# Performance work log

Hardware: AMD Instinct MI355X
Metric: run time of the kernel (lower is better)

The kernel has to match this reference:

```python
import jax, jax.numpy as jnp
import numpy as np

N = 100000        # nodes
E_RAND = 1600000  # random edges (self loops appended -> E = E_RAND + N)
H = 64            # agg_hidden
IN = 7            # in_channels
L = 3             # n_layer
FC = 128          # fc_hidden
C = 2             # num_classes
G = 256           # graphs in the batch
SLOPE = 0.2       # GATv2 LeakyReLU negative slope


def _gatv2(x, src, dst, Wl, bl, Wr, br, att, bias):
    # GATv2Conv, heads=1, concat=True, no edge_attr
    xl = x @ Wl.T + bl                                      # [N,H] source transform
    xr = x @ Wr.T + br                                      # [N,H] target transform
    e = jax.nn.leaky_relu(xl[src] + xr[dst], SLOPE) @ att   # [E] per-edge score
    m = jax.ops.segment_max(e, dst, num_segments=N)         # segment softmax over in-edges
    w = jnp.exp(e - m[dst])
    denom = jax.ops.segment_sum(w, dst, num_segments=N)
    alpha = w / denom[dst]                                  # self loops guarantee denom > 0
    out = jax.ops.segment_sum(alpha[:, None] * xl[src], dst, num_segments=N)
    return out + bias


def _forward(x, eps, m0, v0, mrest, vrest, fc1_W, fc1_b, fc2_W, fc2_b, edge_index, batch):
    src, dst = edge_index[0], edge_index[1]
    mean = jax.nn.elu(_gatv2(x, src, dst, *m0))
    log_var = jax.nn.elu(_gatv2(x, src, dst, *v0))
    for i in range(L - 1):  # dropout is a no-op in eval mode
        mean = jax.nn.elu(_gatv2(mean, src, dst, *[p[i] for p in mrest]))
        log_var = jax.nn.elu(_gatv2(log_var, src, dst, *[p[i] for p in vrest]))
    z = mean + eps * jnp.exp(0.5 * log_var)                 # reparameterize
    counts = jax.ops.segment_sum(jnp.ones((N,), z.dtype), batch, num_segments=G)
    zg = jax.ops.segment_sum(z, batch, num_segments=G) / counts[:, None]  # global_mean_pool
    h = jax.nn.relu(zg @ fc1_W.T + fc1_b)
    logits = h @ fc2_W.T + fc2_b
    return jax.nn.log_softmax(logits, axis=1), mean, log_var


def setup_inputs() -> dict:
    key = jax.random.key(0)
    ks = iter(jax.random.split(key, 48))

    def nrm(shape, s=0.1):
        return s * jax.random.normal(next(ks), shape, jnp.float32)

    x = jax.random.normal(next(ks), (N, IN), jnp.float32)
    src = jax.random.randint(next(ks), (E_RAND,), 0, N)
    dst = jax.random.randint(next(ks), (E_RAND,), 0, N)
    loops = jnp.arange(N)
    edge_index = jnp.stack([jnp.concatenate([src, loops]),
                            jnp.concatenate([dst, loops])])  # add_self_loops=True
    batch = jnp.sort(jax.random.randint(next(ks), (N,), 0, G))
    eps = jax.random.normal(next(ks), (N, H), jnp.float32)

    d = dict(x=x, eps=eps, edge_index=edge_index, batch=batch)
    for pre, din in (("m0", IN), ("v0", IN)):
        d[pre + "_Wl"] = nrm((H, din)); d[pre + "_bl"] = nrm((H,))
        d[pre + "_Wr"] = nrm((H, din)); d[pre + "_br"] = nrm((H,))
        d[pre + "_att"] = nrm((H,));    d[pre + "_bias"] = nrm((H,))
    for pre in ("m", "v"):  # stacked hidden layers [L-1, ...]
        d[pre + "_Wl"] = nrm((L - 1, H, H)); d[pre + "_bl"] = nrm((L - 1, H))
        d[pre + "_Wr"] = nrm((L - 1, H, H)); d[pre + "_br"] = nrm((L - 1, H))
        d[pre + "_att"] = nrm((L - 1, H));   d[pre + "_bias"] = nrm((L - 1, H))
    d["fc1_W"] = nrm((FC, H)); d["fc1_b"] = nrm((FC,))
    d["fc2_W"] = nrm((C, FC)); d["fc2_b"] = nrm((C,))
    return d


def reference(x, eps, edge_index, batch,
              m0_Wl, m0_bl, m0_Wr, m0_br, m0_att, m0_bias,
              v0_Wl, v0_bl, v0_Wr, v0_br, v0_att, v0_bias,
              m_Wl, m_bl, m_Wr, m_br, m_att, m_bias,
              v_Wl, v_bl, v_Wr, v_br, v_att, v_bias,
              fc1_W, fc1_b, fc2_W, fc2_b):
    m0 = (m0_Wl, m0_bl, m0_Wr, m0_br, m0_att, m0_bias)
    v0 = (v0_Wl, v0_bl, v0_Wr, v0_br, v0_att, v0_bias)
    mrest = (m_Wl, m_bl, m_Wr, m_br, m_att, m_bias)
    vrest = (v_Wl, v_bl, v_Wr, v_br, v_att, v_bias)
    return _forward(x, eps, m0, v0, mrest, vrest, fc1_W, fc1_b, fc2_W, fc2_b, edge_index, batch)
```

## Files before the change

kernel.cpp:

```cpp
#include <hip/hip_runtime.h>
#include <hip/hip_fp16.h>
#include <math.h>


#define BSH 7
#define BMSK ((1 << BSH) - 1)
#define CHUNK 4096
#define SNB 4096

typedef _Float16 h2 __attribute__((ext_vector_type(2)));
typedef _Float16 h8 __attribute__((ext_vector_type(8)));
typedef float f4 __attribute__((ext_vector_type(4)));

__device__ __forceinline__ float elu1(float v) {
    return v > 0.f ? v : (__expf(v) - 1.f);
}
__device__ __forceinline__ h2 lrelu2(h2 v) {
    int ai = (*(int*)&v) & 0x7FFF7FFF;
    h2 a = *(h2*)&ai;
    h2 c06 = {(_Float16)0.6f, (_Float16)0.6f};
    h2 c04 = {(_Float16)0.4f, (_Float16)0.4f};
    return v * c06 + a * c04;
}


__global__ void k_hist_bucket(const int* __restrict__ dst, int E,
                              int* __restrict__ bcnt, int nbk) {
    __shared__ int h[1024];
    for (int i = threadIdx.x; i < 1024; i += blockDim.x) h[i] = 0;
    __syncthreads();
    int stride = gridDim.x * blockDim.x;
    for (int e = blockIdx.x * blockDim.x + threadIdx.x; e < E; e += stride)
        atomicAdd(&h[dst[e] >> BSH], 1);
    __syncthreads();
    for (int i = threadIdx.x; i < nbk; i += blockDim.x)
        if (h[i]) atomicAdd(&bcnt[i], h[i]);
}

__global__ void k_scan_buckets(const int* __restrict__ bcnt, int nbk, int* __restrict__ boff) {
    __shared__ int sh[1024];
    int t = threadIdx.x;
    int v = (t < nbk) ? bcnt[t] : 0;
    sh[t] = v;
    __syncthreads();
    for (int o = 1; o < 1024; o <<= 1) {
        int u = (t >= o) ? sh[t - o] : 0;
        __syncthreads();
        sh[t] += u;
        __syncthreads();
    }
    if (t < nbk) boff[t] = sh[t] - v;
    if (t == nbk - 1) boff[nbk] = sh[t];
}

__global__ __launch_bounds__(256) void k_binfill(
    const int* __restrict__ src, const int* __restrict__ dst, int E,
    const int* __restrict__ boff, int* __restrict__ bfill, int* __restrict__ pairs) {
    __shared__ int h[1024];
    __shared__ int sbase[1024];
    int c0 = blockIdx.x * CHUNK;
    int c1 = min(c0 + CHUNK, E);
    for (int i = threadIdx.x; i < 1024; i += 256) h[i] = 0;
    __syncthreads();
    for (int e = c0 + threadIdx.x; e < c1; e += 256)
        atomicAdd(&h[dst[e] >> BSH], 1);
    __syncthreads();
    for (int i = threadIdx.x; i < 1024; i += 256) {
        int c = h[i];
        sbase[i] = c ? (boff[i] + atomicAdd(&bfill[i], c)) : 0;
        h[i] = 0;
    }
    __syncthreads();
    for (int e = c0 + threadIdx.x; e < c1; e += 256) {
        int d = dst[e];
        int b = d >> BSH;
        int off = atomicAdd(&h[b], 1);
        pairs[sbase[b] + off] = (src[e] << BSH) | (d & BMSK);
    }
}

__global__ __launch_bounds__(256) void k_bucket_csr(
    const int* __restrict__ pairs, const int* __restrict__ boff,
    int* __restrict__ rowptr, int* __restrict__ col, int N, int E) {
    __shared__ int deg[128], fill[128], scan[128], base[128];
    int b = blockIdx.x;
    int e0 = boff[b], e1 = boff[b + 1];
    int t = threadIdx.x;
    if (t < 128) { deg[t] = 0; fill[t] = 0; }
    __syncthreads();
    for (int i = e0 + t; i < e1; i += 256)
        atomicAdd(&deg[pairs[i] & BMSK], 1);
    __syncthreads();
    if (t < 128) scan[t] = deg[t];
    __syncthreads();
    for (int o = 1; o < 128; o <<= 1) {
        int u = (t >= o && t < 128) ? scan[t - o] : 0;
        __syncthreads();
        if (t < 128) scan[t] += u;
        __syncthreads();
    }
    if (t < 128) {
        int excl = e0 + scan[t] - deg[t];
        int node = (b << BSH) + t;
        if (node < N) rowptr[node] = excl;
        if (node == N - 1) rowptr[N] = E;
        base[t] = excl;
    }
    __syncthreads();
    for (int i = e0 + t; i < e1; i += 256) {
        int pk = pairs[i];
        int d = pk & BMSK;
        int pos = base[d] + atomicAdd(&fill[d], 1);
        col[pos] = ((unsigned)pk) >> BSH;
    }
}


__global__ __launch_bounds__(256) void k_deg_hist(const int* __restrict__ rowptr, int n,
                                                  int* __restrict__ bin_cnt,
                                                  int* __restrict__ blk_base) {
    __shared__ int h[256];
    h[threadIdx.x] = 0;
    __syncthreads();
    int b0 = blockIdx.x * SNB;
    int b1 = min(b0 + SNB, n);
    for (int i = b0 + threadIdx.x; i < b1; i += 256) {
        int d = 255 - min(rowptr[i + 1] - rowptr[i], 255);
        atomicAdd(&h[d], 1);
    }
    __syncthreads();
    int c = h[threadIdx.x];
    blk_base[blockIdx.x * 256 + threadIdx.x] = c ? atomicAdd(&bin_cnt[threadIdx.x], c) : 0;
}

__global__ void k_scan256(const int* __restrict__ bin_cnt, int* __restrict__ bin_off) {
    __shared__ int sh[256];
    int t = threadIdx.x;
    int v = bin_cnt[t];
    sh[t] = v;
    __syncthreads();
    for (int o = 1; o < 256; o <<= 1) {
        int u = (t >= o) ? sh[t - o] : 0;
        __syncthreads();
        sh[t] += u;
        __syncthreads();
    }
    bin_off[t] = sh[t] - v;
}

__global__ __launch_bounds__(256) void k_deg_scatter(const int* __restrict__ rowptr, int n,
                                                     const int* __restrict__ bin_off,
                                                     const int* __restrict__ blk_base,
                                                     int* __restrict__ nodeof) {
    __shared__ int h[256];
    h[threadIdx.x] = 0;
    __syncthreads();
    int b0 = blockIdx.x * SNB;
    int b1 = min(b0 + SNB, n);
    for (int i = b0 + threadIdx.x; i < b1; i += 256) {
        int d = 255 - min(rowptr[i + 1] - rowptr[i], 255);
        int my = atomicAdd(&h[d], 1);
        nodeof[bin_off[d] + blk_base[blockIdx.x * 256 + d] + my] = i;
    }
}


__global__ void k_transform7(const float* __restrict__ X,
                             const float* __restrict__ mWl, const float* __restrict__ mbl,
                             const float* __restrict__ mWr, const float* __restrict__ mbr,
                             const float* __restrict__ vWl, const float* __restrict__ vbl,
                             const float* __restrict__ vWr, const float* __restrict__ vbr,
                             __half* __restrict__ xlb, __half* __restrict__ xrb, int n) {
    int t = blockIdx.x * blockDim.x + threadIdx.x;
    int node = t >> 6;
    if (node >= n) return;
    int h = t & 63;
    float aml = mbl[h], amr = mbr[h], avl = vbl[h], avr = vbr[h];
#pragma unroll
    for (int k = 0; k < 7; ++k) {
        float xv = X[node * 7 + k];
        aml = fmaf(xv, mWl[h * 7 + k], aml);
        amr = fmaf(xv, mWr[h * 7 + k], amr);
        avl = fmaf(xv, vWl[h * 7 + k], avl);
        avr = fmaf(xv, vWr[h * 7 + k], avr);
    }
    size_t o = (size_t)node * 128;
    xlb[o + h] = __float2half(aml);
    xlb[o + 64 + h] = __float2half(avl);
    xrb[o + h] = __float2half(amr);
    xrb[o + 64 + h] = __float2half(avr);
}

__global__ __launch_bounds__(256) void k_transform_mfma2(
    const float* __restrict__ Xm, const float* __restrict__ Xv,
    const float* __restrict__ mWl, const float* __restrict__ mbl,
    const float* __restrict__ mWr, const float* __restrict__ mbr,
    const float* __restrict__ vWl, const float* __restrict__ vbl,
    const float* __restrict__ vWr, const float* __restrict__ vbr,
    __half* __restrict__ xlb, __half* __restrict__ xrb, int n) {
    int brn = blockIdx.y;
    const float* X  = brn ? Xv : Xm;
    const float* Wl = brn ? vWl : mWl;
    const float* bl = brn ? vbl : mbl;
    const float* Wr = brn ? vWr : mWr;
    const float* br = brn ? vbr : mbr;
    int base = brn * 64;

    __shared__ float biasLds[128];
    {
        int t = threadIdx.x;
        if (t < 64) biasLds[t] = bl[t];
        else if (t < 128) biasLds[t] = br[t - 64];
    }
    __syncthreads();
    int lane = threadIdx.x & 63;
    int l16 = lane & 15, lhi = lane >> 4;

    h8 aW[2][8];
    const float* Wp0 = Wl + (size_t)l16 * 64 + lhi * 8;
    const float* Wp1 = Wr + (size_t)l16 * 64 + lhi * 8;
#pragma unroll
    for (int tl = 0; tl < 4; ++tl) {
#pragma unroll
        for (int c = 0; c < 2; ++c) {
            const float* p0 = Wp0 + (size_t)tl * 16 * 64 + c * 32;
            const float* p1 = Wp1 + (size_t)tl * 16 * 64 + c * 32;
            float4 u0 = *(const float4*)p0, u1 = *(const float4*)(p0 + 4);
            float4 v0 = *(const float4*)p1, v1 = *(const float4*)(p1 + 4);
            h8 a0 = {(_Float16)u0.x, (_Float16)u0.y, (_Float16)u0.z, (_Float16)u0.w,
                     (_Float16)u1.x, (_Float16)u1.y, (_Float16)u1.z, (_Float16)u1.w};
            h8 a1 = {(_Float16)v0.x, (_Float16)v0.y, (_Float16)v0.z, (_Float16)v0.w,
                     (_Float16)v1.x, (_Float16)v1.y, (_Float16)v1.z, (_Float16)v1.w};
            aW[0][tl * 2 + c] = a0;
            aW[1][tl * 2 + c] = a1;
        }
    }

    int ntiles = (n + 15) >> 4;
    int wtile = blockIdx.x * 4 + (threadIdx.x >> 6);
    int wstride = gridDim.x * 4;
    for (int tile = wtile; tile < ntiles; tile += wstride) {
        int nb = tile * 16;
        int node = nb + l16;
        int nload = min(node, n - 1);
        h8 Bf[2];
#pragma unroll
        for (int c = 0; c < 2; ++c) {
            const float* p = X + (size_t)nload * 64 + c * 32 + lhi * 8;
            float4 u0 = *(const float4*)p, u1 = *(const float4*)(p + 4);
            h8 b = {(_Float16)u0.x, (_Float16)u0.y, (_Float16)u0.z, (_Float16)u0.w,
                    (_Float16)u1.x, (_Float16)u1.y, (_Float16)u1.z, (_Float16)u1.w};
            Bf[c] = b;
        }
        f4 acc[2][4];
#pragma unroll
        for (int m = 0; m < 2; ++m)
#pragma unroll
            for (int tl = 0; tl < 4; ++tl) {
                f4 a = {0.f, 0.f, 0.f, 0.f};
                a = __builtin_amdgcn_mfma_f32_16x16x32_f16(aW[m][tl * 2 + 0], Bf[0], a, 0, 0, 0);
                a = __builtin_amdgcn_mfma_f32_16x16x32_f16(aW[m][tl * 2 + 1], Bf[1], a, 0, 0, 0);
                acc[m][tl] = a;
            }
        if (node < n) {
#pragma unroll
            for (int m = 0; m < 2; ++m) {
                __half* op = (m ? xrb : xlb) + (size_t)node * 128 + base;
#pragma unroll
                for (int tl = 0; tl < 4; ++tl) {
                    float4 bb = *(const float4*)&biasLds[m * 64 + tl * 16 + 4 * lhi];
                    h2 lo = {(_Float16)(acc[m][tl][0] + bb.x), (_Float16)(acc[m][tl][1] + bb.y)};
                    h2 hi = {(_Float16)(acc[m][tl][2] + bb.z), (_Float16)(acc[m][tl][3] + bb.w)};
                    uint2 pk = {*(unsigned*)&lo, *(unsigned*)&hi};
                    *(uint2*)(op + tl * 16 + 4 * lhi) = pk;
                }
            }
        }
    }
}


__global__ __launch_bounds__(256) void k_aggregate2(
    const __half* __restrict__ xlb, const __half* __restrict__ xrb,
    const float* __restrict__ attm, const float* __restrict__ attv,
    const float* __restrict__ biasm, const float* __restrict__ biasv,
    const int* __restrict__ rowptr, const int* __restrict__ col,
    const int* __restrict__ nodeof,
    float* __restrict__ outm, float* __restrict__ outv, int n) {
    int t = blockIdx.x * blockDim.x + threadIdx.x;
    int gid = t >> 4;
    if (gid >= n) return;
    int node = nodeof[gid];
    int l = t & 15;
    int s = l & 7;
    bool isv = l >= 8;

    int4 xri = ((const int4*)(xrb + (size_t)node * 128))[l];
    h2 xr0 = *(h2*)&xri.x, xr1 = *(h2*)&xri.y, xr2 = *(h2*)&xri.z, xr3 = *(h2*)&xri.w;
    const float* ap = (isv ? attv : attm) + s * 8;
    float4 af0 = *(const float4*)ap, af1 = *(const float4*)(ap + 4);
    h2 a0 = {(_Float16)af0.x, (_Float16)af0.y}, a1 = {(_Float16)af0.z, (_Float16)af0.w};
    h2 a2 = {(_Float16)af1.x, (_Float16)af1.y}, a3 = {(_Float16)af1.z, (_Float16)af1.w};

    float ac0 = 0.f, ac1 = 0.f, ac2 = 0.f, ac3 = 0.f;
    float ac4 = 0.f, ac5 = 0.f, ac6 = 0.f, ac7 = 0.f;
    float ssum = 0.f;

    auto proc = [&](int4 qi) {
        h2 x0 = *(h2*)&qi.x, x1 = *(h2*)&qi.y, x2 = *(h2*)&qi.z, x3 = *(h2*)&qi.w;
        h2 p = lrelu2(x0 + xr0) * a0;
        p = lrelu2(x1 + xr1) * a1 + p;
        p = lrelu2(x2 + xr2) * a2 + p;
        p = lrelu2(x3 + xr3) * a3 + p;
        float sc = (float)p.x + (float)p.y;
        sc += __shfl_xor(sc, 1);
        sc += __shfl_xor(sc, 2);
        sc += __shfl_xor(sc, 4);
        float w = __expf(sc);
        ssum += w;
        ac0 = fmaf(w, (float)x0.x, ac0);
        ac1 = fmaf(w, (float)x0.y, ac1);
        ac2 = fmaf(w, (float)x1.x, ac2);
        ac3 = fmaf(w, (float)x1.y, ac3);
        ac4 = fmaf(w, (float)x2.x, ac4);
        ac5 = fmaf(w, (float)x2.y, ac5);
        ac6 = fmaf(w, (float)x3.x, ac6);
        ac7 = fmaf(w, (float)x3.y, ac7);
    };

    int r0 = rowptr[node], r1 = rowptr[node + 1];
    int e = r0;
    for (; e + 7 < r1; e += 8) {
        int sn0 = col[e],     sn1 = col[e + 1], sn2 = col[e + 2], sn3 = col[e + 3];
        int sn4 = col[e + 4], sn5 = col[e + 5], sn6 = col[e + 6], sn7 = col[e + 7];
        int4 q0 = ((const int4*)(xlb + (size_t)sn0 * 128))[l];
        int4 q1 = ((const int4*)(xlb + (size_t)sn1 * 128))[l];
        int4 q2 = ((const int4*)(xlb + (size_t)sn2 * 128))[l];
        int4 q3 = ((const int4*)(xlb + (size_t)sn3 * 128))[l];
        int4 q4 = ((const int4*)(xlb + (size_t)sn4 * 128))[l];
        int4 q5 = ((const int4*)(xlb + (size_t)sn5 * 128))[l];
        int4 q6 = ((const int4*)(xlb + (size_t)sn6 * 128))[l];
        int4 q7 = ((const int4*)(xlb + (size_t)sn7 * 128))[l];
        proc(q0); proc(q1); proc(q2); proc(q3);
        proc(q4); proc(q5); proc(q6); proc(q7);
    }
    for (; e + 3 < r1; e += 4) {
        int sn0 = col[e], sn1 = col[e + 1], sn2 = col[e + 2], sn3 = col[e + 3];
        int4 q0 = ((const int4*)(xlb + (size_t)sn0 * 128))[l];
        int4 q1 = ((const int4*)(xlb + (size_t)sn1 * 128))[l];
        int4 q2 = ((const int4*)(xlb + (size_t)sn2 * 128))[l];
        int4 q3 = ((const int4*)(xlb + (size_t)sn3 * 128))[l];
        proc(q0); proc(q1); proc(q2); proc(q3);
    }
    for (; e < r1; ++e) {
        int sn = col[e];
        proc(((const int4*)(xlb + (size_t)sn * 128))[l]);
    }

    float inv = 1.f / ssum;
    const float* bp = (isv ? biasv : biasm) + s * 8;
    float4 b0 = *(const float4*)bp, b1 = *(const float4*)(bp + 4);
    float* op = (isv ? outv : outm) + (size_t)node * 64 + s * 8;
    float4 r0v, r1v;
    r0v.x = elu1(fmaf(ac0, inv, b0.x));
    r0v.y = elu1(fmaf(ac1, inv, b0.y));
    r0v.z = elu1(fmaf(ac2, inv, b0.z));
    r0v.w = elu1(fmaf(ac3, inv, b0.w));
    r1v.x = elu1(fmaf(ac4, inv, b1.x));
    r1v.y = elu1(fmaf(ac5, inv, b1.y));
    r1v.z = elu1(fmaf(ac6, inv, b1.z));
    r1v.w = elu1(fmaf(ac7, inv, b1.w));
    *(float4*)op = r0v;
    *(float4*)(op + 4) = r1v;
}


__global__ void k_zpool(const float* __restrict__ mean, const float* __restrict__ logvar,
                        const float* __restrict__ eps, const int* __restrict__ batch,
                        float* __restrict__ zsum, float* __restrict__ cnt, int n) {
    int wave = blockIdx.x * 4 + (threadIdx.x >> 6);
    int lane = threadIdx.x & 63;
    int n0 = wave * 16;
    if (n0 >= n) return;
    int n1 = min(n0 + 16, n);
    float acc = 0.f, c = 0.f;
    int gcur = -1;
    for (int nd = n0; nd < n1; ++nd) {
        int g = batch[nd];
        if (g != gcur) {
            if (gcur >= 0) {
                atomicAdd(&zsum[gcur * 64 + lane], acc);
                if (lane == 0) atomicAdd(&cnt[gcur], c);
            }
            gcur = g; acc = 0.f; c = 0.f;
        }
        size_t o = (size_t)nd * 64 + lane;
        float z = fmaf(eps[o], __expf(0.5f * logvar[o]), mean[o]);
        acc += z;
        c += 1.f;
    }
    if (gcur >= 0) {
        atomicAdd(&zsum[gcur * 64 + lane], acc);
        if (lane == 0) atomicAdd(&cnt[gcur], c);
    }
}


__global__ void k_fchead(const float* __restrict__ zsum, const float* __restrict__ cnt,
                         const float* __restrict__ fc1W, const float* __restrict__ fc1b,
                         const float* __restrict__ fc2W, const float* __restrict__ fc2b,
                         float* __restrict__ out) {
    __shared__ float zg[64];
    __shared__ float h1[128];
    __shared__ float lg[2];
    int g = blockIdx.x;
    int t = threadIdx.x;
    if (t < 64) zg[t] = zsum[g * 64 + t] / cnt[g];
    __syncthreads();
    float h = fc1b[t];
#pragma unroll
    for (int k = 0; k < 64; ++k) h = fmaf(zg[k], fc1W[t * 64 + k], h);
    h1[t] = fmaxf(h, 0.f);
    __syncthreads();
    if (t < 2) {
        float l = fc2b[t];
        for (int k = 0; k < 128; ++k) l = fmaf(h1[k], fc2W[t * 128 + k], l);
        lg[t] = l;
    }
    __syncthreads();
    if (t == 0) {
        float mx = fmaxf(lg[0], lg[1]);
        float lse = mx + logf(expf(lg[0] - mx) + expf(lg[1] - mx));
        out[g * 2 + 0] = lg[0] - lse;
        out[g * 2 + 1] = lg[1] - lse;
    }
}


extern "C" void kernel_launch(void* const* d_in, const int* in_sizes, int n_in,
                              void* d_out, int out_size, void* d_ws, size_t ws_size,
                              hipStream_t stream) {
    const float* x     = (const float*)d_in[0];
    const float* eps   = (const float*)d_in[1];
    const int*   eidx  = (const int*)d_in[2];
    const int*   batch = (const int*)d_in[3];
    const float* m0_Wl = (const float*)d_in[4];
    const float* m0_bl = (const float*)d_in[5];
    const float* m0_Wr = (const float*)d_in[6];
    const float* m0_br = (const float*)d_in[7];
    const float* m0_att = (const float*)d_in[8];
    const float* m0_bias = (const float*)d_in[9];
    const float* v0_Wl = (const float*)d_in[10];
    const float* v0_bl = (const float*)d_in[11];
    const float* v0_Wr = (const float*)d_in[12];
    const float* v0_br = (const float*)d_in[13];
    const float* v0_att = (const float*)d_in[14];
    const float* v0_bias = (const float*)d_in[15];
    const float* m_Wl = (const float*)d_in[16];
    const float* m_bl = (const float*)d_in[17];
    const float* m_Wr = (const float*)d_in[18];
    const float* m_br = (const float*)d_in[19];
    const float* m_att = (const float*)d_in[20];
    const float* m_bias = (const float*)d_in[21];
    const float* v_Wl = (const float*)d_in[22];
    const float* v_bl = (const float*)d_in[23];
    const float* v_Wr = (const float*)d_in[24];
    const float* v_br = (const float*)d_in[25];
    const float* v_att = (const float*)d_in[26];
    const float* v_bias = (const float*)d_in[27];
    const float* fc1W = (const float*)d_in[28];
    const float* fc1b = (const float*)d_in[29];
    const float* fc2W = (const float*)d_in[30];
    const float* fc2b = (const float*)d_in[31];

    const int N = in_sizes[1] / 64;
    const int E = in_sizes[2] / 2;
    const int G = (out_size - N * 128) / 2;
    const int nbk = (N + (1 << BSH) - 1) >> BSH;
    const int nsb = (N + SNB - 1) / SNB;
    const int* srcp = eidx;
    const int* dstp = eidx + E;

    char* wsb = (char*)d_ws;
    size_t off = 0;
    auto carve = [&](size_t bytes) -> void* {
        void* p = wsb + off;
        off += (bytes + 255) & ~(size_t)255;
        return p;
    };
    int*    rowptr   = (int*)carve((size_t)(N + 1) * sizeof(int));
    int*    col      = (int*)carve((size_t)E * sizeof(int));
    int*    pairs    = (int*)carve((size_t)E * sizeof(int));
    int*    bcnt     = (int*)carve((size_t)(nbk + 1) * sizeof(int));
    int*    boff     = (int*)carve((size_t)(nbk + 1) * sizeof(int));
    int*    bfill    = (int*)carve((size_t)nbk * sizeof(int));
    int*    nodeof   = (int*)carve((size_t)N * sizeof(int));
    int*    bin_cnt  = (int*)carve(256 * sizeof(int));
    int*    bin_off  = (int*)carve(256 * sizeof(int));
    int*    blk_base = (int*)carve((size_t)nsb * 256 * sizeof(int));
    __half* xlb      = (__half*)carve((size_t)N * 128 * sizeof(__half));
    __half* xrb      = (__half*)carve((size_t)N * 128 * sizeof(__half));
    float*  zsum     = (float*)carve((size_t)G * 64 * sizeof(float));
    float*  cnt      = (float*)carve((size_t)G * sizeof(float));
    (void)ws_size;

    float* out_logits = (float*)d_out;
    float* mean_buf   = out_logits + (size_t)G * 2;
    float* logvar_buf = mean_buf + (size_t)N * 64;

    const int agrid = (N * 16 + 255) / 256;
    const int tgrid7 = (N * 64 + 255) / 256;
    const int mgrid = ((N + 15) / 16 + 3) / 4;
    const int zgrid = ((N + 15) / 16 + 3) / 4;

    (void)hipMemsetAsync(bcnt, 0, (size_t)nbk * sizeof(int), stream);
    (void)hipMemsetAsync(bfill, 0, (size_t)nbk * sizeof(int), stream);
    (void)hipMemsetAsync(bin_cnt, 0, 256 * sizeof(int), stream);
    (void)hipMemsetAsync(zsum, 0, (size_t)G * 64 * sizeof(float), stream);
    (void)hipMemsetAsync(cnt, 0, (size_t)G * sizeof(float), stream);
    k_hist_bucket<<<256, 256, 0, stream>>>(dstp, E, bcnt, nbk);
    k_scan_buckets<<<1, 1024, 0, stream>>>(bcnt, nbk, boff);
    k_binfill<<<(E + CHUNK - 1) / CHUNK, 256, 0, stream>>>(srcp, dstp, E, boff, bfill, pairs);
    k_bucket_csr<<<nbk, 256, 0, stream>>>(pairs, boff, rowptr, col, N, E);

    k_deg_hist<<<nsb, 256, 0, stream>>>(rowptr, N, bin_cnt, blk_base);
    k_scan256<<<1, 256, 0, stream>>>(bin_cnt, bin_off);
    k_deg_scatter<<<nsb, 256, 0, stream>>>(rowptr, N, bin_off, blk_base, nodeof);

    k_transform7<<<tgrid7, 256, 0, stream>>>(x, m0_Wl, m0_bl, m0_Wr, m0_br,
                                             v0_Wl, v0_bl, v0_Wr, v0_br, xlb, xrb, N);
    k_aggregate2<<<agrid, 256, 0, stream>>>(xlb, xrb, m0_att, v0_att, m0_bias, v0_bias,
                                            rowptr, col, nodeof, mean_buf, logvar_buf, N);

    for (int l = 0; l < 2; ++l) {
        k_transform_mfma2<<<dim3(mgrid, 2), 256, 0, stream>>>(
            mean_buf, logvar_buf,
            m_Wl + (size_t)l * 4096, m_bl + l * 64, m_Wr + (size_t)l * 4096, m_br + l * 64,
            v_Wl + (size_t)l * 4096, v_bl + l * 64, v_Wr + (size_t)l * 4096, v_br + l * 64,
            xlb, xrb, N);
        k_aggregate2<<<agrid, 256, 0, stream>>>(xlb, xrb, m_att + l * 64, v_att + l * 64,
                                                m_bias + l * 64, v_bias + l * 64,
                                                rowptr, col, nodeof, mean_buf, logvar_buf, N);
    }

    k_zpool<<<zgrid, 256, 0, stream>>>(mean_buf, logvar_buf, eps, batch, zsum, cnt, N);
    k_fchead<<<G, 128, 0, stream>>>(zsum, cnt, fc1W, fc1b, fc2W, fc2b, out_logits);
}
```

Measured before the change: 487.3 us.

## Software-pipeline neighbor gathers and use fdot2, DPP reductions and exp2 in GATv2 aggregation

The edge aggregation loop is restructured into a double-buffered software pipeline: the next four neighbor feature rows and column indices are prefetched while the current four are processed, replacing the 8/4/1 unrolled loops. The score computation splits leaky ReLU into 0.6*y + 0.4*|y| dot products via fp32-accumulating fdot2, folds log2(e) into the attention weights so exp2 can be used, and replaces the shfl_xor reductions with DPP lane permutes. The aim is to hide gather latency and cut ALU and cross-lane cost per edge, at the cost of more registers and a different rounding path for the scores.

Result: no change. 485.0 us (-0.5%).

```diff
diff --git a/kernel.cpp b/kernel.cpp
--- a/kernel.cpp
+++ b/kernel.cpp
@@ -15,12 +15,35 @@
 __device__ __forceinline__ float elu1(float v) {
     return v > 0.f ? v : (__expf(v) - 1.f);
 }
-__device__ __forceinline__ h2 lrelu2(h2 v) {
-    int ai = (*(int*)&v) & 0x7FFF7FFF;
-    h2 a = *(h2*)&ai;
-    h2 c06 = {(_Float16)0.6f, (_Float16)0.6f};
-    h2 c04 = {(_Float16)0.4f, (_Float16)0.4f};
-    return v * c06 + a * c04;
+
+__device__ __forceinline__ float exp2fast(float x) {
+#if defined(__has_builtin)
+#if __has_builtin(__builtin_amdgcn_exp2f)
+    return __builtin_amdgcn_exp2f(x);
+#else
+    return exp2f(x);
+#endif
+#else
+    return exp2f(x);
+#endif
+}
+
+__device__ __forceinline__ float dot2f(h2 a, h2 b, float c) {
+#if defined(__has_builtin)
+#if __has_builtin(__builtin_amdgcn_fdot2)
+    return __builtin_amdgcn_fdot2(a, b, c, false);
+#else
+    return fmaf((float)a.x, (float)b.x, fmaf((float)a.y, (float)b.y, c));
+#endif
+#else
+    return fmaf((float)a.x, (float)b.x, fmaf((float)a.y, (float)b.y, c));
+#endif
+}
+
+template <int CTRL>
+__device__ __forceinline__ float dppf(float v) {
+    int r = __builtin_amdgcn_update_dpp(0, __builtin_bit_cast(int, v), CTRL, 0xF, 0xF, true);
+    return __builtin_bit_cast(float, r);
 }
 
 
@@ -299,8 +322,16 @@
     h2 xr0 = *(h2*)&xri.x, xr1 = *(h2*)&xri.y, xr2 = *(h2*)&xri.z, xr3 = *(h2*)&xri.w;
     const float* ap = (isv ? attv : attm) + s * 8;
     float4 af0 = *(const float4*)ap, af1 = *(const float4*)(ap + 4);
-    h2 a0 = {(_Float16)af0.x, (_Float16)af0.y}, a1 = {(_Float16)af0.z, (_Float16)af0.w};
-    h2 a2 = {(_Float16)af1.x, (_Float16)af1.y}, a3 = {(_Float16)af1.z, (_Float16)af1.w};
+    const float C6 = 0.6f * 1.44269504f;
+    const float C4 = 0.4f * 1.44269504f;
+    h2 a6_0 = {(_Float16)(af0.x * C6), (_Float16)(af0.y * C6)};
+    h2 a6_1 = {(_Float16)(af0.z * C6), (_Float16)(af0.w * C6)};
+    h2 a6_2 = {(_Float16)(af1.x * C6), (_Float16)(af1.y * C6)};
+    h2 a6_3 = {(_Float16)(af1.z * C6), (_Float16)(af1.w * C6)};
+    h2 a4_0 = {(_Float16)(af0.x * C4), (_Float16)(af0.y * C4)};
+    h2 a4_1 = {(_Float16)(af0.z * C4), (_Float16)(af0.w * C4)};
+    h2 a4_2 = {(_Float16)(af1.x * C4), (_Float16)(af1.y * C4)};
+    h2 a4_3 = {(_Float16)(af1.z * C4), (_Float16)(af1.w * C4)};
 
     float ac0 = 0.f, ac1 = 0.f, ac2 = 0.f, ac3 = 0.f;
     float ac4 = 0.f, ac5 = 0.f, ac6 = 0.f, ac7 = 0.f;
@@ -308,15 +339,25 @@
 
     auto proc = [&](int4 qi) {
         h2 x0 = *(h2*)&qi.x, x1 = *(h2*)&qi.y, x2 = *(h2*)&qi.z, x3 = *(h2*)&qi.w;
-        h2 p = lrelu2(x0 + xr0) * a0;
-        p = lrelu2(x1 + xr1) * a1 + p;
-        p = lrelu2(x2 + xr2) * a2 + p;
-        p = lrelu2(x3 + xr3) * a3 + p;
-        float sc = (float)p.x + (float)p.y;
-        sc += __shfl_xor(sc, 1);
-        sc += __shfl_xor(sc, 2);
-        sc += __shfl_xor(sc, 4);
-        float w = __expf(sc);
+        h2 y0 = x0 + xr0, y1 = x1 + xr1, y2 = x2 + xr2, y3 = x3 + xr3;
+        int z0i = (*(int*)&y0) & 0x7FFF7FFF;
+        int z1i = (*(int*)&y1) & 0x7FFF7FFF;
+        int z2i = (*(int*)&y2) & 0x7FFF7FFF;
+        int z3i = (*(int*)&y3) & 0x7FFF7FFF;
+        h2 z0 = *(h2*)&z0i, z1 = *(h2*)&z1i, z2 = *(h2*)&z2i, z3 = *(h2*)&z3i;
+        float sc = dot2f(y0, a6_0, 0.f);
+        float sa = dot2f(z0, a4_0, 0.f);
+        sc = dot2f(y1, a6_1, sc);
+        sa = dot2f(z1, a4_1, sa);
+        sc = dot2f(y2, a6_2, sc);
+        sa = dot2f(z2, a4_2, sa);
+        sc = dot2f(y3, a6_3, sc);
+        sa = dot2f(z3, a4_3, sa);
+        sc += sa;
+        sc += dppf<0xB1>(sc);
+        sc += dppf<0x4E>(sc);
+        sc += dppf<0x141>(sc);
+        float w = exp2fast(sc);
         ssum += w;
         ac0 = fmaf(w, (float)x0.x, ac0);
         ac1 = fmaf(w, (float)x0.y, ac1);
@@ -329,33 +370,36 @@
     };
 
     int r0 = rowptr[node], r1 = rowptr[node + 1];
+    const int4* xp = (const int4*)xlb + l;
+    int last = r1 - 1;
+    int nb = (r1 - r0) >> 2;
     int e = r0;
-    for (; e + 7 < r1; e += 8) {
-        int sn0 = col[e],     sn1 = col[e + 1], sn2 = col[e + 2], sn3 = col[e + 3];
-        int sn4 = col[e + 4], sn5 = col[e + 5], sn6 = col[e + 6], sn7 = col[e + 7];
-        int4 q0 = ((const int4*)(xlb + (size_t)sn0 * 128))[l];
-        int4 q1 = ((const int4*)(xlb + (size_t)sn1 * 128))[l];
-        int4 q2 = ((const int4*)(xlb + (size_t)sn2 * 128))[l];
-        int4 q3 = ((const int4*)(xlb + (size_t)sn3 * 128))[l];
-        int4 q4 = ((const int4*)(xlb + (size_t)sn4 * 128))[l];
-        int4 q5 = ((const int4*)(xlb + (size_t)sn5 * 128))[l];
-        int4 q6 = ((const int4*)(xlb + (size_t)sn6 * 128))[l];
-        int4 q7 = ((const int4*)(xlb + (size_t)sn7 * 128))[l];
-        proc(q0); proc(q1); proc(q2); proc(q3);
-        proc(q4); proc(q5); proc(q6); proc(q7);
-    }
-    for (; e + 3 < r1; e += 4) {
-        int sn0 = col[e], sn1 = col[e + 1], sn2 = col[e + 2], sn3 = col[e + 3];
-        int4 q0 = ((const int4*)(xlb + (size_t)sn0 * 128))[l];
-        int4 q1 = ((const int4*)(xlb + (size_t)sn1 * 128))[l];
-        int4 q2 = ((const int4*)(xlb + (size_t)sn2 * 128))[l];
-        int4 q3 = ((const int4*)(xlb + (size_t)sn3 * 128))[l];
-        proc(q0); proc(q1); proc(q2); proc(q3);
-    }
-    for (; e < r1; ++e) {
-        int sn = col[e];
-        proc(((const int4*)(xlb + (size_t)sn * 128))[l]);
-    }
+    int t0 = 0, t1 = 0, t2 = 0, t3 = 0;
+    int4 qA0, qA1, qA2, qA3;
+    if (nb) {
+        int s0 = col[e], s1 = col[e + 1], s2 = col[e + 2], s3 = col[e + 3];
+        qA0 = xp[(size_t)s0 * 16]; qA1 = xp[(size_t)s1 * 16];
+        qA2 = xp[(size_t)s2 * 16]; qA3 = xp[(size_t)s3 * 16];
+        int p = e + 4;
+        t0 = col[min(p, last)];     t1 = col[min(p + 1, last)];
+        t2 = col[min(p + 2, last)]; t3 = col[min(p + 3, last)];
+    }
+    for (int b = 0; b < nb; ++b) {
+        int4 qB0, qB1, qB2, qB3;
+        bool more = (b + 1 < nb);
+        if (more) {
+            qB0 = xp[(size_t)t0 * 16]; qB1 = xp[(size_t)t1 * 16];
+            qB2 = xp[(size_t)t2 * 16]; qB3 = xp[(size_t)t3 * 16];
+            int p = e + 8;
+            t0 = col[min(p, last)];     t1 = col[min(p + 1, last)];
+            t2 = col[min(p + 2, last)]; t3 = col[min(p + 3, last)];
+        }
+        proc(qA0); proc(qA1); proc(qA2); proc(qA3);
+        if (more) { qA0 = qB0; qA1 = qB1; qA2 = qB2; qA3 = qB3; }
+        e += 4;
+    }
+    for (e = r0 + nb * 4; e < r1; ++e)
+        proc(xp[(size_t)col[e] * 16]);
 
     float inv = 1.f / ssum;
     const float* bp = (isv ? biasv : biasm) + s * 8;
```
